# Performance work log

Measured on AMD Instinct MI355X. Metric: run time of the kernel, lower is better.

Reference implementation:

```python
import jax, jax.numpy as jnp
import numpy as np

N, E, D = 50000, 600000, 128
EPS = 1e-8
BALL_EPS = 1e-5  # keep norms strictly < 1 for artanh


def _logmap0(x):
    # Poincare ball, c=1: logmap0(x) = artanh(||x||) * x / ||x||
    nrm = jnp.linalg.norm(x, axis=-1, keepdims=True)
    nrm_c = jnp.clip(nrm, EPS, 1.0 - BALL_EPS)
    return jnp.arctanh(nrm_c) * x / nrm_c


def _expmap0(v):
    # Poincare ball, c=1: expmap0(v) = tanh(||v||) * v / ||v||
    nrm = jnp.linalg.norm(v, axis=-1, keepdims=True)
    nrm_c = jnp.maximum(nrm, EPS)
    return jnp.tanh(nrm_c) * v / nrm_c


def setup_inputs() -> dict:
    key = jax.random.key(0)
    ks = jax.random.split(key, 7)
    # node features scaled to lie well inside the unit ball (valid Poincare points)
    x = jax.random.normal(ks[0], (N, D), dtype=jnp.float32) * 0.01
    edge_index = jax.random.randint(ks[1], (2, E), 0, N, dtype=jnp.int32)
    s = 1.0 / np.sqrt(D)
    w_msg1 = jax.random.normal(ks[2], (D, D), dtype=jnp.float32) * s
    w_msg2 = jax.random.normal(ks[3], (D, D), dtype=jnp.float32) * s
    w_upd1 = jax.random.normal(ks[4], (D, D), dtype=jnp.float32) * s
    w_upd2 = jax.random.normal(ks[5], (D, D), dtype=jnp.float32) * s
    b = lambda: jnp.zeros((D,), dtype=jnp.float32)
    return {"x": x, "edge_index": edge_index,
            "w_msg1": w_msg1, "b_msg1": b(), "w_msg2": w_msg2, "b_msg2": b(),
            "w_upd1": w_upd1, "b_upd1": b(), "w_upd2": w_upd2, "b_upd2": b()}


def reference(x, edge_index, w_msg1, b_msg1, w_msg2, b_msg2,
              w_upd1, b_upd1, w_upd2, b_upd2):
    x_t = _logmap0(x)                                  # [N, D]
    row, col = edge_index[0], edge_index[1]            # dst, src
    h = x_t[col]                                       # gather [E, D]
    msgs = jax.nn.relu(h @ w_msg1 + b_msg1) @ w_msg2 + b_msg2   # [E, D]
    # mean aggregation: scatter-add then divide by in-degree
    summed = jax.ops.segment_sum(msgs, row, num_segments=N)      # [N, D]
    count = jax.ops.segment_sum(jnp.ones((E,), dtype=jnp.float32), row, num_segments=N)
    out = summed / (count[:, None] + EPS)
    out = jax.nn.relu(out @ w_upd1 + b_upd1) @ w_upd2 + b_upd2
    return _expmap0(out)
```

## Files before the change

### kernel.cpp

```cpp
#include <hip/hip_runtime.h>
#include <hip/hip_bf16.h>


#define DD 128
#define CAP 32

typedef __attribute__((ext_vector_type(8))) short short8;
typedef __attribute__((ext_vector_type(4))) float f32x4;

__device__ __forceinline__ unsigned short f2bf(float f) {
  unsigned u = __float_as_uint(f);
  u += 0x7fffu + ((u >> 16) & 1u);
  return (unsigned short)(u >> 16);
}
__device__ __forceinline__ float bf2f(short h) {
  return __uint_as_float(((unsigned)(unsigned short)h) << 16);
}

__global__ void k_init(const float* __restrict__ w1, const float* __restrict__ w2,
                       const float* __restrict__ w3, const float* __restrict__ w4,
                       unsigned short* __restrict__ P, int* __restrict__ degv, int N) {
  if (blockIdx.x < 32) {
    int idx = blockIdx.x * 256 + threadIdx.x;
    int m = idx >> 11;
    int id = idx & 2047;
    int f = id >> 6, l = id & 63;
    int cc = f >> 2, s = f & 3, q = l >> 4, n15 = l & 15;
    const float* W = (m == 0) ? w1 : (m == 1) ? w2 : (m == 2) ? w3 : w4;
    const float* wp = W + (s * 32 + q * 8) * DD + cc * 16 + n15;
    unsigned short* op = P + (size_t)m * 16384 + (size_t)id * 8;
#pragma unroll
    for (int j = 0; j < 8; ++j) op[j] = f2bf(wp[j * DD]);
  } else {
    int i = (blockIdx.x - 32) * 256 + threadIdx.x;
    if (i < N) degv[i] = 0;
  }
}

__global__ __launch_bounds__(256) void k_stage1(
    const float* __restrict__ x, const int* __restrict__ ei,
    const unsigned short* __restrict__ Pa, const float* __restrict__ ba,
    const unsigned short* __restrict__ Pb, const float* __restrict__ bb,
    unsigned short* __restrict__ node_msg, int* __restrict__ degv,
    int* __restrict__ ebuf, int N, int E, int nf) {
  __shared__ unsigned short As[32 * 136];
  const int tid = threadIdx.x;

  if (blockIdx.x >= nf) {
    int e = (blockIdx.x - nf) * 256 + tid;
    if (e < E) {
      int dst = ei[e];
      int srcn = ei[E + e];
      int pos = atomicAdd(degv + dst, 1);
      if (pos < CAP) ebuf[(size_t)dst * CAP + pos] = srcn;
    }
    return;
  }

  const int lane = tid & 63;
  const int wv = tid >> 6;
  const int rt = wv >> 1;
  const int ct = wv & 1;
  const int q = lane >> 4;
  const int n15 = lane & 15;
  const int row0 = blockIdx.x * 32;
  const int g = (wv << 2) | q;

#pragma unroll
  for (int i = 0; i < 2; ++i) {
    const int r = g * 2 + i;
    const int grow = row0 + r;
    f32x4 s0 = {0.f, 0.f, 0.f, 0.f}, s1 = {0.f, 0.f, 0.f, 0.f};
    if (grow < N) {
      const f32x4* p = (const f32x4*)(x + (size_t)grow * DD + n15 * 8);
      s0 = p[0];
      s1 = p[1];
      float ss = s0[0]*s0[0] + s0[1]*s0[1] + s0[2]*s0[2] + s0[3]*s0[3]
               + s1[0]*s1[0] + s1[1]*s1[1] + s1[2]*s1[2] + s1[3]*s1[3];
      ss += __shfl_xor(ss, 1);
      ss += __shfl_xor(ss, 2);
      ss += __shfl_xor(ss, 4);
      ss += __shfl_xor(ss, 8);
      float nrm = sqrtf(ss);
      float nc = fminf(fmaxf(nrm, 1e-8f), 1.0f - 1e-5f);
      float sc = atanhf(nc) / nc;
      s0 *= sc;
      s1 *= sc;
    }
    uint4 pk;
    pk.x = (unsigned)f2bf(s0[0]) | ((unsigned)f2bf(s0[1]) << 16);
    pk.y = (unsigned)f2bf(s0[2]) | ((unsigned)f2bf(s0[3]) << 16);
    pk.z = (unsigned)f2bf(s1[0]) | ((unsigned)f2bf(s1[1]) << 16);
    pk.w = (unsigned)f2bf(s1[2]) | ((unsigned)f2bf(s1[3]) << 16);
    *(uint4*)((unsigned*)As + r * 68 + n15 * 4) = pk;
  }
  __syncthreads();

  float bc[4];
#pragma unroll
  for (int c = 0; c < 4; ++c) bc[c] = ba[ct * 64 + c * 16 + n15];
  f32x4 acc[4];
#pragma unroll
  for (int c = 0; c < 4; ++c) acc[c] = (f32x4){0.f, 0.f, 0.f, 0.f};
  const int abase = (rt * 16 + n15) * 136 + q * 8;
#pragma unroll
  for (int s = 0; s < 4; ++s) {
    short8 a = *(const short8*)&As[abase + s * 32];
#pragma unroll
    for (int c = 0; c < 4; ++c) {
      short8 b = *(const short8*)&Pa[(size_t)(((((ct << 2) | c) << 2) | s) * 64 + lane) * 8];
      acc[c] = __builtin_amdgcn_mfma_f32_16x16x32_bf16(a, b, acc[c], 0, 0, 0);
    }
  }
  __syncthreads();

#pragma unroll
  for (int c = 0; c < 4; ++c)
#pragma unroll
    for (int rr = 0; rr < 4; ++rr) {
      float v = fmaxf(acc[c][rr] + bc[c], 0.f);
      As[(rt * 16 + q * 4 + rr) * 136 + ct * 64 + c * 16 + n15] = f2bf(v);
    }
  __syncthreads();

#pragma unroll
  for (int c = 0; c < 4; ++c) bc[c] = bb[ct * 64 + c * 16 + n15];
#pragma unroll
  for (int c = 0; c < 4; ++c) acc[c] = (f32x4){0.f, 0.f, 0.f, 0.f};
#pragma unroll
  for (int s = 0; s < 4; ++s) {
    short8 a = *(const short8*)&As[abase + s * 32];
#pragma unroll
    for (int c = 0; c < 4; ++c) {
      short8 b = *(const short8*)&Pb[(size_t)(((((ct << 2) | c) << 2) | s) * 64 + lane) * 8];
      acc[c] = __builtin_amdgcn_mfma_f32_16x16x32_bf16(a, b, acc[c], 0, 0, 0);
    }
  }

  __syncthreads();
#pragma unroll
  for (int c = 0; c < 4; ++c)
#pragma unroll
    for (int rr = 0; rr < 4; ++rr)
      As[(rt * 16 + q * 4 + rr) * 136 + ct * 64 + c * 16 + n15] =
          f2bf(acc[c][rr] + bc[c]);
  __syncthreads();
#pragma unroll
  for (int k = 0; k < 2; ++k) {
    int u = tid + k * 256;
    int r = u >> 4, ch = u & 15;
    int grow = row0 + r;
    if (grow < N)
      *(short8*)(node_msg + (size_t)grow * DD + ch * 8) =
          *(const short8*)&As[r * 136 + ch * 8];
  }
}

__global__ __launch_bounds__(256) void k_stage2(
    const unsigned short* __restrict__ node_msg, const int* __restrict__ degv,
    const int* __restrict__ ebuf, const unsigned short* __restrict__ Pa,
    const float* __restrict__ ba, const unsigned short* __restrict__ Pb,
    const float* __restrict__ bb, float* __restrict__ out, int N) {
  __shared__ unsigned short As[32 * 136];
  __shared__ float nrmb[64];
  const int tid = threadIdx.x;
  const int lane = tid & 63;
  const int wv = tid >> 6;
  const int rt = wv >> 1;
  const int ct = wv & 1;
  const int q = lane >> 4;
  const int n15 = lane & 15;
  const int row0 = blockIdx.x * 32;
  const int g = (wv << 2) | q;

#pragma unroll
  for (int i = 0; i < 2; ++i) {
    const int r = g * 2 + i;
    const int grow = row0 + r;
    f32x4 s0 = {0.f, 0.f, 0.f, 0.f}, s1 = {0.f, 0.f, 0.f, 0.f};
    if (grow < N) {
      const int d = degv[grow];
      const int dl = (d < CAP) ? d : CAP;
      const int* eb = ebuf + (size_t)grow * CAP;
      f32x4 t0 = {0.f, 0.f, 0.f, 0.f}, t1 = {0.f, 0.f, 0.f, 0.f};
      int t = 0;
      for (; t + 7 < dl; t += 8) {
        int4 ia = *(const int4*)(eb + t);
        int4 ib = *(const int4*)(eb + t + 4);
        short8 v0 = *(const short8*)(node_msg + (size_t)ia.x * DD + n15 * 8);
        short8 v1 = *(const short8*)(node_msg + (size_t)ia.y * DD + n15 * 8);
        short8 v2 = *(const short8*)(node_msg + (size_t)ia.z * DD + n15 * 8);
        short8 v3 = *(const short8*)(node_msg + (size_t)ia.w * DD + n15 * 8);
        short8 v4 = *(const short8*)(node_msg + (size_t)ib.x * DD + n15 * 8);
        short8 v5 = *(const short8*)(node_msg + (size_t)ib.y * DD + n15 * 8);
        short8 v6 = *(const short8*)(node_msg + (size_t)ib.z * DD + n15 * 8);
        short8 v7 = *(const short8*)(node_msg + (size_t)ib.w * DD + n15 * 8);
#pragma unroll
        for (int j = 0; j < 4; ++j) {
          s0[j] += bf2f(v0[j]) + bf2f(v1[j]);
          s1[j] += bf2f(v0[j + 4]) + bf2f(v1[j + 4]);
          t0[j] += bf2f(v2[j]) + bf2f(v3[j]);
          t1[j] += bf2f(v2[j + 4]) + bf2f(v3[j + 4]);
          s0[j] += bf2f(v4[j]) + bf2f(v5[j]);
          s1[j] += bf2f(v4[j + 4]) + bf2f(v5[j + 4]);
          t0[j] += bf2f(v6[j]) + bf2f(v7[j]);
          t1[j] += bf2f(v6[j + 4]) + bf2f(v7[j + 4]);
        }
      }
      if (t + 3 < dl) {
        int4 ia = *(const int4*)(eb + t);
        short8 v0 = *(const short8*)(node_msg + (size_t)ia.x * DD + n15 * 8);
        short8 v1 = *(const short8*)(node_msg + (size_t)ia.y * DD + n15 * 8);
        short8 v2 = *(const short8*)(node_msg + (size_t)ia.z * DD + n15 * 8);
        short8 v3 = *(const short8*)(node_msg + (size_t)ia.w * DD + n15 * 8);
#pragma unroll
        for (int j = 0; j < 4; ++j) {
          s0[j] += bf2f(v0[j]) + bf2f(v1[j]);
          s1[j] += bf2f(v0[j + 4]) + bf2f(v1[j + 4]);
          t0[j] += bf2f(v2[j]) + bf2f(v3[j]);
          t1[j] += bf2f(v2[j + 4]) + bf2f(v3[j + 4]);
        }
        t += 4;
      }
      for (; t < dl; ++t) {
        int sa = eb[t];
        short8 va = *(const short8*)(node_msg + (size_t)sa * DD + n15 * 8);
#pragma unroll
        for (int j = 0; j < 4; ++j) {
          s0[j] += bf2f(va[j]);
          s1[j] += bf2f(va[j + 4]);
        }
      }
      s0 += t0;
      s1 += t1;
      float inv = 1.f / ((float)d + 1e-8f);
      s0 *= inv;
      s1 *= inv;
    }
    uint4 pk;
    pk.x = (unsigned)f2bf(s0[0]) | ((unsigned)f2bf(s0[1]) << 16);
    pk.y = (unsigned)f2bf(s0[2]) | ((unsigned)f2bf(s0[3]) << 16);
    pk.z = (unsigned)f2bf(s1[0]) | ((unsigned)f2bf(s1[1]) << 16);
    pk.w = (unsigned)f2bf(s1[2]) | ((unsigned)f2bf(s1[3]) << 16);
    *(uint4*)((unsigned*)As + r * 68 + n15 * 4) = pk;
  }
  __syncthreads();

  float bc[4];
#pragma unroll
  for (int c = 0; c < 4; ++c) bc[c] = ba[ct * 64 + c * 16 + n15];
  f32x4 acc[4];
#pragma unroll
  for (int c = 0; c < 4; ++c) acc[c] = (f32x4){0.f, 0.f, 0.f, 0.f};
  const int abase = (rt * 16 + n15) * 136 + q * 8;
#pragma unroll
  for (int s = 0; s < 4; ++s) {
    short8 a = *(const short8*)&As[abase + s * 32];
#pragma unroll
    for (int c = 0; c < 4; ++c) {
      short8 b = *(const short8*)&Pa[(size_t)(((((ct << 2) | c) << 2) | s) * 64 + lane) * 8];
      acc[c] = __builtin_amdgcn_mfma_f32_16x16x32_bf16(a, b, acc[c], 0, 0, 0);
    }
  }
  __syncthreads();

#pragma unroll
  for (int c = 0; c < 4; ++c)
#pragma unroll
    for (int rr = 0; rr < 4; ++rr) {
      float v = fmaxf(acc[c][rr] + bc[c], 0.f);
      As[(rt * 16 + q * 4 + rr) * 136 + ct * 64 + c * 16 + n15] = f2bf(v);
    }
  __syncthreads();

#pragma unroll
  for (int c = 0; c < 4; ++c) bc[c] = bb[ct * 64 + c * 16 + n15];
#pragma unroll
  for (int c = 0; c < 4; ++c) acc[c] = (f32x4){0.f, 0.f, 0.f, 0.f};
#pragma unroll
  for (int s = 0; s < 4; ++s) {
    short8 a = *(const short8*)&As[abase + s * 32];
#pragma unroll
    for (int c = 0; c < 4; ++c) {
      short8 b = *(const short8*)&Pb[(size_t)(((((ct << 2) | c) << 2) | s) * 64 + lane) * 8];
      acc[c] = __builtin_amdgcn_mfma_f32_16x16x32_bf16(a, b, acc[c], 0, 0, 0);
    }
  }

  float v[4][4];
#pragma unroll
  for (int rr = 0; rr < 4; ++rr) {
    float ssq = 0.f;
#pragma unroll
    for (int c = 0; c < 4; ++c) {
      v[c][rr] = acc[c][rr] + bc[c];
      ssq += v[c][rr] * v[c][rr];
    }
    ssq += __shfl_xor(ssq, 1);
    ssq += __shfl_xor(ssq, 2);
    ssq += __shfl_xor(ssq, 4);
    ssq += __shfl_xor(ssq, 8);
    if (n15 == 0) nrmb[(rt * 16 + q * 4 + rr) * 2 + ct] = ssq;
  }
  __syncthreads();
#pragma unroll
  for (int rr = 0; rr < 4; ++rr) {
    int r = rt * 16 + q * 4 + rr;
    int grow = row0 + r;
    float ssq = nrmb[r * 2] + nrmb[r * 2 + 1];
    float nrm = sqrtf(ssq);
    float nc = fmaxf(nrm, 1e-8f);
    float sc = tanhf(nc) / nc;
    if (grow < N) {
#pragma unroll
      for (int c = 0; c < 4; ++c)
        out[(size_t)grow * DD + ct * 64 + c * 16 + n15] = v[c][rr] * sc;
    }
  }
}

extern "C" void kernel_launch(void* const* d_in, const int* in_sizes, int n_in,
                              void* d_out, int out_size, void* d_ws, size_t ws_size,
                              hipStream_t stream) {
  const float* x = (const float*)d_in[0];
  const int* ei = (const int*)d_in[1];
  const float* w1 = (const float*)d_in[2];
  const float* b1 = (const float*)d_in[3];
  const float* w2 = (const float*)d_in[4];
  const float* b2 = (const float*)d_in[5];
  const float* w3 = (const float*)d_in[6];
  const float* b3 = (const float*)d_in[7];
  const float* w4 = (const float*)d_in[8];
  const float* b4 = (const float*)d_in[9];
  const int N = in_sizes[0] / DD;
  const int E = in_sizes[1] / 2;
  const int nf = (N + 31) / 32;
  const int ne = (E + 255) / 256;

  unsigned short* node_msg = (unsigned short*)d_ws;
  int* degv = (int*)(node_msg + (size_t)N * DD);
  int* ebuf = degv + N;
  uintptr_t pw = (uintptr_t)(ebuf + (size_t)N * CAP);
  pw = (pw + 63) & ~(uintptr_t)63;
  unsigned short* P = (unsigned short*)pw;
  float* outp = (float*)d_out;

  hipLaunchKernelGGL(k_init, dim3(32 + (N + 255) / 256), dim3(256), 0, stream,
                     w1, w2, w3, w4, P, degv, N);
  hipLaunchKernelGGL(k_stage1, dim3(nf + ne), dim3(256), 0, stream,
                     x, ei, P, b1, P + 16384, b2, node_msg, degv, ebuf, N, E, nf);
  hipLaunchKernelGGL(k_stage2, dim3(nf), dim3(256), 0, stream,
                     node_msg, degv, ebuf, P + 2 * 16384, b3, P + 3 * 16384, b4,
                     outp, N);
}
```

Before: 183.9 us.

## Merge three kernels into one cooperative persistent kernel with grid syncs

Replaces the init, stage1 and stage2 launches with a single cooperative kernel sized from occupancy, where blocks loop over tiles and phases are separated by grid.sync(). The edge-fill work now handles two edges per thread and is interleaved with the first MLP tiles in one persistent loop. The aim is to remove inter-kernel launch gaps and tail effects. In exchange it adds grid-wide barrier cost, depends on the queried occupancy for grid size (capped at 2048 blocks), and adds a block barrier after each tile.

```diff
diff --git a/kernel.cpp b/kernel.cpp
--- a/kernel.cpp
+++ b/kernel.cpp
@@ -1,5 +1,8 @@
 #include <hip/hip_runtime.h>
+#include <hip/hip_cooperative_groups.h>
 #include <hip/hip_bf16.h>
+
+namespace cg = cooperative_groups;
 
 
 #define DD 128
@@ -17,53 +20,19 @@
   return __uint_as_float(((unsigned)(unsigned short)h) << 16);
 }
 
-__global__ void k_init(const float* __restrict__ w1, const float* __restrict__ w2,
-                       const float* __restrict__ w3, const float* __restrict__ w4,
-                       unsigned short* __restrict__ P, int* __restrict__ degv, int N) {
-  if (blockIdx.x < 32) {
-    int idx = blockIdx.x * 256 + threadIdx.x;
-    int m = idx >> 11;
-    int id = idx & 2047;
-    int f = id >> 6, l = id & 63;
-    int cc = f >> 2, s = f & 3, q = l >> 4, n15 = l & 15;
-    const float* W = (m == 0) ? w1 : (m == 1) ? w2 : (m == 2) ? w3 : w4;
-    const float* wp = W + (s * 32 + q * 8) * DD + cc * 16 + n15;
-    unsigned short* op = P + (size_t)m * 16384 + (size_t)id * 8;
-#pragma unroll
-    for (int j = 0; j < 8; ++j) op[j] = f2bf(wp[j * DD]);
-  } else {
-    int i = (blockIdx.x - 32) * 256 + threadIdx.x;
-    if (i < N) degv[i] = 0;
-  }
-}
-
-__global__ __launch_bounds__(256) void k_stage1(
-    const float* __restrict__ x, const int* __restrict__ ei,
-    const unsigned short* __restrict__ Pa, const float* __restrict__ ba,
-    const unsigned short* __restrict__ Pb, const float* __restrict__ bb,
-    unsigned short* __restrict__ node_msg, int* __restrict__ degv,
-    int* __restrict__ ebuf, int N, int E, int nf) {
-  __shared__ unsigned short As[32 * 136];
+__device__ __forceinline__ void mlp1_tile(
+    int t, const float* __restrict__ x, const unsigned short* __restrict__ Pa,
+    const float* __restrict__ ba, const unsigned short* __restrict__ Pb,
+    const float* __restrict__ bb, unsigned short* __restrict__ node_msg, int N,
+    unsigned short* As) {
   const int tid = threadIdx.x;
-
-  if (blockIdx.x >= nf) {
-    int e = (blockIdx.x - nf) * 256 + tid;
-    if (e < E) {
-      int dst = ei[e];
-      int srcn = ei[E + e];
-      int pos = atomicAdd(degv + dst, 1);
-      if (pos < CAP) ebuf[(size_t)dst * CAP + pos] = srcn;
-    }
-    return;
-  }
-
   const int lane = tid & 63;
   const int wv = tid >> 6;
   const int rt = wv >> 1;
   const int ct = wv & 1;
   const int q = lane >> 4;
   const int n15 = lane & 15;
-  const int row0 = blockIdx.x * 32;
+  const int row0 = t * 32;
   const int g = (wv << 2) | q;
 
 #pragma unroll
@@ -154,15 +123,15 @@
       *(short8*)(node_msg + (size_t)grow * DD + ch * 8) =
           *(const short8*)&As[r * 136 + ch * 8];
   }
-}
-
-__global__ __launch_bounds__(256) void k_stage2(
-    const unsigned short* __restrict__ node_msg, const int* __restrict__ degv,
-    const int* __restrict__ ebuf, const unsigned short* __restrict__ Pa,
-    const float* __restrict__ ba, const unsigned short* __restrict__ Pb,
-    const float* __restrict__ bb, float* __restrict__ out, int N) {
-  __shared__ unsigned short As[32 * 136];
-  __shared__ float nrmb[64];
+  __syncthreads();
+}
+
+__device__ __forceinline__ void stage2_tile(
+    int t, const unsigned short* __restrict__ node_msg,
+    const int* __restrict__ degv, const int* __restrict__ ebuf,
+    const unsigned short* __restrict__ Pa, const float* __restrict__ ba,
+    const unsigned short* __restrict__ Pb, const float* __restrict__ bb,
+    float* __restrict__ out, int N, unsigned short* As, float* nrmb) {
   const int tid = threadIdx.x;
   const int lane = tid & 63;
   const int wv = tid >> 6;
@@ -170,7 +139,7 @@
   const int ct = wv & 1;
   const int q = lane >> 4;
   const int n15 = lane & 15;
-  const int row0 = blockIdx.x * 32;
+  const int row0 = t * 32;
   const int g = (wv << 2) | q;
 
 #pragma unroll
@@ -183,10 +152,10 @@
       const int dl = (d < CAP) ? d : CAP;
       const int* eb = ebuf + (size_t)grow * CAP;
       f32x4 t0 = {0.f, 0.f, 0.f, 0.f}, t1 = {0.f, 0.f, 0.f, 0.f};
-      int t = 0;
-      for (; t + 7 < dl; t += 8) {
-        int4 ia = *(const int4*)(eb + t);
-        int4 ib = *(const int4*)(eb + t + 4);
+      int tt = 0;
+      for (; tt + 7 < dl; tt += 8) {
+        int4 ia = *(const int4*)(eb + tt);
+        int4 ib = *(const int4*)(eb + tt + 4);
         short8 v0 = *(const short8*)(node_msg + (size_t)ia.x * DD + n15 * 8);
         short8 v1 = *(const short8*)(node_msg + (size_t)ia.y * DD + n15 * 8);
         short8 v2 = *(const short8*)(node_msg + (size_t)ia.z * DD + n15 * 8);
@@ -207,8 +176,8 @@
           t1[j] += bf2f(v6[j + 4]) + bf2f(v7[j + 4]);
         }
       }
-      if (t + 3 < dl) {
-        int4 ia = *(const int4*)(eb + t);
+      if (tt + 3 < dl) {
+        int4 ia = *(const int4*)(eb + tt);
         short8 v0 = *(const short8*)(node_msg + (size_t)ia.x * DD + n15 * 8);
         short8 v1 = *(const short8*)(node_msg + (size_t)ia.y * DD + n15 * 8);
         short8 v2 = *(const short8*)(node_msg + (size_t)ia.z * DD + n15 * 8);
@@ -220,10 +189,10 @@
           t0[j] += bf2f(v2[j]) + bf2f(v3[j]);
           t1[j] += bf2f(v2[j + 4]) + bf2f(v3[j + 4]);
         }
-        t += 4;
+        tt += 4;
       }
-      for (; t < dl; ++t) {
-        int sa = eb[t];
+      for (; tt < dl; ++tt) {
+        int sa = eb[tt];
         short8 va = *(const short8*)(node_msg + (size_t)sa * DD + n15 * 8);
 #pragma unroll
         for (int j = 0; j < 4; ++j) {
@@ -317,6 +286,65 @@
         out[(size_t)grow * DD + ct * 64 + c * 16 + n15] = v[c][rr] * sc;
     }
   }
+  __syncthreads();
+}
+
+__global__ __launch_bounds__(256) void k_mega(
+    const float* __restrict__ x, const int* __restrict__ ei,
+    const float* __restrict__ w1, const float* __restrict__ w2,
+    const float* __restrict__ w3, const float* __restrict__ w4,
+    const float* __restrict__ b1, const float* __restrict__ b2,
+    const float* __restrict__ b3, const float* __restrict__ b4,
+    unsigned short* __restrict__ P, int* __restrict__ degv,
+    int* __restrict__ ebuf, unsigned short* __restrict__ node_msg,
+    float* __restrict__ out, int N, int E, int nfill, int nmlp) {
+  __shared__ unsigned short As[32 * 136];
+  __shared__ float nrmb[64];
+  cg::grid_group grid = cg::this_grid();
+  const int tid = threadIdx.x;
+  const int bid = blockIdx.x;
+  const int gsz = gridDim.x;
+
+  const int nzero = (N + 255) >> 8;
+  for (int u = bid; u < 32 + nzero; u += gsz) {
+    if (u < 32) {
+      int idx = u * 256 + tid;
+      int m = idx >> 11, id = idx & 2047;
+      int f = id >> 6, l = id & 63;
+      int cc = f >> 2, s = f & 3, q = l >> 4, n15 = l & 15;
+      const float* W = (m == 0) ? w1 : (m == 1) ? w2 : (m == 2) ? w3 : w4;
+      const float* wp = W + (s * 32 + q * 8) * DD + cc * 16 + n15;
+      unsigned short* op = P + (size_t)m * 16384 + (size_t)id * 8;
+#pragma unroll
+      for (int j = 0; j < 8; ++j) op[j] = f2bf(wp[j * DD]);
+    } else {
+      int i = (u - 32) * 256 + tid;
+      if (i < N) degv[i] = 0;
+    }
+  }
+  grid.sync();
+
+  for (int u = bid; u < nfill + nmlp; u += gsz) {
+    if (u < nfill) {
+      int e = u * 512 + tid;
+#pragma unroll
+      for (int k = 0; k < 2; ++k, e += 256) {
+        if (e < E) {
+          int dst = ei[e];
+          int srcn = ei[E + e];
+          int pos = atomicAdd(degv + dst, 1);
+          if (pos < CAP) ebuf[(size_t)dst * CAP + pos] = srcn;
+        }
+      }
+    } else {
+      mlp1_tile(u - nfill, x, P, b1, P + 16384, b2, node_msg, N, As);
+    }
+  }
+  grid.sync();
+
+  for (int u = bid; u < nmlp; u += gsz)
+    stage2_tile(u, node_msg, degv, ebuf, P + 2 * 16384, b3, P + 3 * 16384, b4,
+                out, N, As, nrmb);
 }
 
 extern "C" void kernel_launch(void* const* d_in, const int* in_sizes, int n_in,
@@ -332,10 +360,10 @@
   const float* b3 = (const float*)d_in[7];
   const float* w4 = (const float*)d_in[8];
   const float* b4 = (const float*)d_in[9];
-  const int N = in_sizes[0] / DD;
-  const int E = in_sizes[1] / 2;
-  const int nf = (N + 31) / 32;
-  const int ne = (E + 255) / 256;
+  int N = in_sizes[0] / DD;
+  int E = in_sizes[1] / 2;
+  int nfill = (E + 511) / 512;
+  int nmlp = (N + 31) / 32;
 
   unsigned short* node_msg = (unsigned short*)d_ws;
   int* degv = (int*)(node_msg + (size_t)N * DD);
@@ -345,11 +373,17 @@
   unsigned short* P = (unsigned short*)pw;
   float* outp = (float*)d_out;
 
-  hipLaunchKernelGGL(k_init, dim3(32 + (N + 255) / 256), dim3(256), 0, stream,
-                     w1, w2, w3, w4, P, degv, N);
-  hipLaunchKernelGGL(k_stage1, dim3(nf + ne), dim3(256), 0, stream,
-                     x, ei, P, b1, P + 16384, b2, node_msg, degv, ebuf, N, E, nf);
-  hipLaunchKernelGGL(k_stage2, dim3(nf), dim3(256), 0, stream,
-                     node_msg, degv, ebuf, P + 2 * 16384, b3, P + 3 * 16384, b4,
-                     outp, N);
-}
+  int occ = 0;
+  if (hipOccupancyMaxActiveBlocksPerMultiprocessor(&occ, (const void*)k_mega,
+                                                   256, 0) != hipSuccess ||
+      occ <= 0)
+    occ = 4;
+  int grid = occ * 256;
+  if (grid > 2048) grid = 2048;
+
+  void* args[] = {&x,  &ei, &w1, &w2, &w3,   &w4,   &b1,       &b2,
+                  &b3, &b4, &P,  &degv, &ebuf, &node_msg, &outp,
+                  &N,  &E,  &nfill, &nmlp};
+  hipLaunchCooperativeKernel((const void*)k_mega, dim3(grid), dim3(256), args,
+                             0, stream);
+}
```

Measured after the change: 300.4 us. +63.4%, slower.
